# Optimization experiments

Hardware: AMD Instinct MI355X
Metric: run time of the kernel (lower is better)

Reference implementation:

```python
import jax, jax.numpy as jnp
import numpy as np

N_HEAD = 16


def setup_inputs() -> dict:
    key = jax.random.key(0)
    ks = jax.random.split(key, 5)
    B, T, D_IN, D = 2, 2048, 1152, 1024
    s_in = 1.0 / np.sqrt(D_IN)
    s_d = 1.0 / np.sqrt(D)
    return {
        "xp": jax.random.normal(ks[0], (B, T, D_IN), jnp.float32),
        "Wq": jax.random.normal(ks[1], (D_IN, D), jnp.float32) * s_in,
        "bq": jnp.zeros((D,), jnp.float32),
        "Wk": jax.random.normal(ks[2], (D_IN, D), jnp.float32) * s_in,
        "bk": jnp.zeros((D,), jnp.float32),
        "Wv": jax.random.normal(ks[3], (D_IN, D), jnp.float32) * s_in,
        "bv": jnp.zeros((D,), jnp.float32),
        "Wp": jax.random.normal(ks[4], (D, D), jnp.float32) * s_d,
        "bp": jnp.zeros((D,), jnp.float32),
    }


def reference(xp, Wq, bq, Wk, bk, Wv, bv, Wp, bp):
    B, T, _ = xp.shape
    D = Wq.shape[1]
    hd = D // N_HEAD  # head dim
    # q, k, v projections -> [B, H, T, hd]
    def split_heads(t):
        return t.reshape(B, T, N_HEAD, hd).transpose(0, 2, 1, 3)
    q = split_heads(xp @ Wq + bq)
    k = split_heads(xp @ Wk + bk)
    v = split_heads(xp @ Wv + bv)
    scale = 1.0 / np.sqrt(hd).astype(np.float32)
    att = jnp.einsum("bhqd,bhkd->bhqk", q, k) * scale  # [B,H,T,T]
    causal = jnp.tril(jnp.ones((T, T), bool))
    att = jnp.where(causal[None, None], att, -jnp.inf)
    att = jax.nn.softmax(att, axis=-1)
    y = jnp.einsum("bhqk,bhkd->bhqd", att, v)  # [B,H,T,hd]
    y = y.transpose(0, 2, 1, 3).reshape(B, T, D)
    return y @ Wp + bp
```

## Files before the change

### kernel.cpp

```cpp
#include <hip/hip_runtime.h>
#include <hip/hip_bf16.h>

typedef __attribute__((ext_vector_type(8))) short bf16x8;
typedef __attribute__((ext_vector_type(4))) float f32x4;
typedef __attribute__((ext_vector_type(2))) unsigned int u32x2;

__device__ __forceinline__ void gload_lds16(const void* g, void* l) {
    __builtin_amdgcn_global_load_lds(
        (const __attribute__((address_space(1))) unsigned int*)g,
        (__attribute__((address_space(3))) unsigned int*)l, 16, 0, 0);
}

__global__ void k_cvt_bf16(const float* __restrict__ x, __hip_bfloat16* __restrict__ o, int n8) {
    int i = blockIdx.x * 256 + threadIdx.x;
    if (i >= n8) return;
    const float4* xp = (const float4*)(x + (size_t)i * 8);
    float4 a = xp[0], b = xp[1];
    union { __hip_bfloat16 h[8]; uint4 u; } tu;
    tu.h[0] = __float2bfloat16(a.x); tu.h[1] = __float2bfloat16(a.y);
    tu.h[2] = __float2bfloat16(a.z); tu.h[3] = __float2bfloat16(a.w);
    tu.h[4] = __float2bfloat16(b.x); tu.h[5] = __float2bfloat16(b.y);
    tu.h[6] = __float2bfloat16(b.z); tu.h[7] = __float2bfloat16(b.w);
    *(uint4*)(o + (size_t)i * 8) = tu.u;
}

__global__ void k_tr(const float* __restrict__ src, __hip_bfloat16* __restrict__ dst, int K, int N) {
    __shared__ float tile[32][33];
    int n0 = blockIdx.x * 32, k0 = blockIdx.y * 32;
    int tx = threadIdx.x & 31, ty = threadIdx.x >> 5;
#pragma unroll
    for (int i = 0; i < 4; i++)
        tile[ty + i * 8][tx] = src[(size_t)(k0 + ty + i * 8) * N + n0 + tx];
    __syncthreads();
#pragma unroll
    for (int i = 0; i < 4; i++)
        dst[(size_t)(n0 + ty + i * 8) * K + k0 + tx] = __float2bfloat16(tile[tx][ty + i * 8]);
}

#define QSCALE 0.18033688011111204f

template <int EPI>
__global__ __launch_bounds__(256, 2) void k_gemm(
    const __hip_bfloat16* __restrict__ A, const __hip_bfloat16* __restrict__ Bt,
    int M, int N, int K,
    const float* __restrict__ b0, const float* __restrict__ b1, const float* __restrict__ b2,
    __hip_bfloat16* __restrict__ qb, __hip_bfloat16* __restrict__ kb, __hip_bfloat16* __restrict__ vb,
    float* __restrict__ outp)
{
    __shared__ __align__(16) __hip_bfloat16 As[128 * 64];
    __shared__ __align__(16) __hip_bfloat16 Bs[128 * 64];
    const int t = threadIdx.x;
    const int lane = t & 63, w = t >> 6;
    const int wr = w >> 1, wc = w & 1;
    const int r16 = lane & 15, kg = lane >> 4;
    const int m0 = blockIdx.x * 128, n0 = blockIdx.y * 128;
    f32x4 acc[4][4] = {};
    const int ksteps = K >> 6;
    for (int kt = 0; kt < ksteps; ++kt) {
        if (kt) __syncthreads();
        const int ks = kt * 64;
#pragma unroll
        for (int i = 0; i < 4; i++) {
            int ci = i * 256 + t;
            int row = ci >> 3, kc = (ci & 7) * 8;
            gload_lds16(A + (size_t)(m0 + row) * K + ks + kc, As + ci * 8);
        }
#pragma unroll
        for (int i = 0; i < 4; i++) {
            int ci = i * 256 + t;
            int row = ci >> 3, kc = (ci & 7) * 8;
            gload_lds16(Bt + (size_t)(n0 + row) * K + ks + kc, Bs + ci * 8);
        }
        __syncthreads();
#pragma unroll
        for (int c = 0; c < 2; c++) {
            bf16x8 af[4], bfr[4];
#pragma unroll
            for (int mi = 0; mi < 4; mi++)
                af[mi] = *(const bf16x8*)(As + (wr * 64 + mi * 16 + r16) * 64 + c * 32 + kg * 8);
#pragma unroll
            for (int ni = 0; ni < 4; ni++)
                bfr[ni] = *(const bf16x8*)(Bs + (wc * 64 + ni * 16 + r16) * 64 + c * 32 + kg * 8);
#pragma unroll
            for (int mi = 0; mi < 4; mi++)
#pragma unroll
                for (int ni = 0; ni < 4; ni++)
                    acc[mi][ni] = __builtin_amdgcn_mfma_f32_16x16x32_bf16(af[mi], bfr[ni], acc[mi][ni], 0, 0, 0);
        }
    }
#pragma unroll
    for (int mi = 0; mi < 4; mi++) {
#pragma unroll
        for (int ni = 0; ni < 4; ni++) {
#pragma unroll
            for (int j = 0; j < 4; j++) {
                int m = m0 + wr * 64 + mi * 16 + kg * 4 + j;
                int n = n0 + wc * 64 + ni * 16 + r16;
                float val = acc[mi][ni][j];
                if (EPI == 0) {
                    int proj = n >> 10, r = n & 1023;
                    int hh = r >> 6, dd = r & 63;
                    int bb = m >> 11, tt = m & 2047;
                    if (proj == 0) {
                        val = (val + b0[r]) * QSCALE;
                        qb[((size_t)(bb * 16 + hh) * 2048 + tt) * 64 + dd] = __float2bfloat16(val);
                    } else if (proj == 1) {
                        val += b1[r];
                        kb[((size_t)(bb * 16 + hh) * 2048 + tt) * 64 + dd] = __float2bfloat16(val);
                    } else {
                        val += b2[r];
                        vb[((size_t)(bb * 16 + hh) * 64 + dd) * 2048 + tt] = __float2bfloat16(val);
                    }
                } else {
                    outp[(size_t)m * N + n] = val + b0[n];
                }
            }
        }
    }
}

__global__ __launch_bounds__(256, 4) void k_attn(
    const __hip_bfloat16* __restrict__ qbuf,
    const __hip_bfloat16* __restrict__ kbuf,
    const __hip_bfloat16* __restrict__ vtbuf,
    __hip_bfloat16* __restrict__ y)
{
    __shared__ __align__(16) __hip_bfloat16 Kl[2][64 * 64];
    __shared__ __align__(16) __hip_bfloat16 Vl[2][64 * 64];
    __shared__ __align__(16) __hip_bfloat16 Pl[4 * 16 * 64];
    const int t = threadIdx.x, lane = t & 63, w = t >> 6;
    const int r16 = lane & 15, kg = lane >> 4;
    const int g = blockIdx.x;
    const int c4 = g >> 8, p = g & 255;
    const int bh = (p >> 5) * 4 + c4;
    const int rr = p & 31;
    const int qt = (c4 & 1) ? rr : 31 - rr;
    const int swr = (r16 & 7) << 3;
    const int q0 = qt * 64 + w * 16;
    const __hip_bfloat16* qp = qbuf + ((size_t)bh * 2048 + q0) * 64;
    bf16x8 qf0 = *(const bf16x8*)(qp + r16 * 64 + kg * 8);
    bf16x8 qf1 = *(const bf16x8*)(qp + r16 * 64 + 32 + kg * 8);
    f32x4 O[4] = {};
    float m_s = -3.0e38f, l_s = 0.f;
    const __hip_bfloat16* kb = kbuf + (size_t)bh * 2048 * 64;
    const __hip_bfloat16* vb = vtbuf + (size_t)bh * 64 * 2048;
    __hip_bfloat16* pw = Pl + w * 16 * 64;

    const int ci0 = t, ci1 = 256 + t;
    const int kr0 = ci0 >> 3, sc0 = ((ci0 & 7) * 8) ^ ((kr0 & 7) << 3);
    const int kr1 = ci1 >> 3, sc1 = ((ci1 & 7) * 8) ^ ((kr1 & 7) << 3);

    gload_lds16(kb + (size_t)kr0 * 64 + sc0, &Kl[0][ci0 * 8]);
    gload_lds16(kb + (size_t)kr1 * 64 + sc1, &Kl[0][ci1 * 8]);
    gload_lds16(vb + (size_t)kr0 * 2048 + sc0, &Vl[0][ci0 * 8]);
    gload_lds16(vb + (size_t)kr1 * 2048 + sc1, &Vl[0][ci1 * 8]);
    __syncthreads();

    for (int kt = 0; kt <= qt; ++kt) {
        const int cur = kt & 1;
        if (kt < qt) {
            const int kn = kt + 1;
            gload_lds16(kb + (size_t)kn * 4096 + (size_t)kr0 * 64 + sc0, &Kl[cur ^ 1][ci0 * 8]);
            gload_lds16(kb + (size_t)kn * 4096 + (size_t)kr1 * 64 + sc1, &Kl[cur ^ 1][ci1 * 8]);
            gload_lds16(vb + (size_t)kr0 * 2048 + kn * 64 + sc0, &Vl[cur ^ 1][ci0 * 8]);
            gload_lds16(vb + (size_t)kr1 * 2048 + kn * 64 + sc1, &Vl[cur ^ 1][ci1 * 8]);
        }
        const __hip_bfloat16* Klb = Kl[cur];
        const __hip_bfloat16* Vlb = Vl[cur];
        f32x4 S[4];
#pragma unroll
        for (int ct = 0; ct < 4; ct++) {
            f32x4 s = {};
            const int r = ct * 16 + r16;
            bf16x8 kf0 = *(const bf16x8*)(Klb + r * 64 + ((kg * 8) ^ swr));
            s = __builtin_amdgcn_mfma_f32_16x16x32_bf16(kf0, qf0, s, 0, 0, 0);
            bf16x8 kf1 = *(const bf16x8*)(Klb + r * 64 + ((32 + kg * 8) ^ swr));
            s = __builtin_amdgcn_mfma_f32_16x16x32_bf16(kf1, qf1, s, 0, 0, 0);
            S[ct] = s;
        }
        if (kt == qt) {
#pragma unroll
            for (int ct = 0; ct < 4; ct++)
#pragma unroll
                for (int j = 0; j < 4; j++)
                    if (ct * 16 + kg * 4 + j > w * 16 + r16) S[ct][j] = -3.0e38f;
        }
        float rmax = S[0][0];
#pragma unroll
        for (int ct = 0; ct < 4; ct++)
#pragma unroll
            for (int j = 0; j < 4; j++) rmax = fmaxf(rmax, S[ct][j]);
        rmax = fmaxf(rmax, __shfl_xor(rmax, 16));
        rmax = fmaxf(rmax, __shfl_xor(rmax, 32));
        if (__any(rmax > m_s + 8.0f)) {
            float mn = fmaxf(m_s, rmax);
            float alpha_s = exp2f(m_s - mn);
            m_s = mn;
            l_s *= alpha_s;
#pragma unroll
            for (int j = 0; j < 4; j++) {
                float aj = __shfl(alpha_s, (lane & 48) | (kg * 4 + j));
#pragma unroll
                for (int ot = 0; ot < 4; ot++) O[ot][j] *= aj;
            }
        }
        float rsum = 0.f;
#pragma unroll
        for (int ct = 0; ct < 4; ct++)
#pragma unroll
            for (int j = 0; j < 4; j++) {
                S[ct][j] = exp2f(S[ct][j] - m_s);
                rsum += S[ct][j];
            }
        rsum += __shfl_xor(rsum, 16);
        rsum += __shfl_xor(rsum, 32);
        l_s += rsum;
#pragma unroll
        for (int ct = 0; ct < 4; ct++) {
            union { __hip_bfloat16 h[4]; u32x2 u; } pk;
            pk.h[0] = __float2bfloat16(S[ct][0]);
            pk.h[1] = __float2bfloat16(S[ct][1]);
            pk.h[2] = __float2bfloat16(S[ct][2]);
            pk.h[3] = __float2bfloat16(S[ct][3]);
            const int col = (ct * 16 + kg * 4) ^ swr;
            *(u32x2*)(pw + r16 * 64 + col) = pk.u;
        }
        bf16x8 pa0 = *(const bf16x8*)(pw + r16 * 64 + ((kg * 8) ^ swr));
        bf16x8 pa1 = *(const bf16x8*)(pw + r16 * 64 + ((32 + kg * 8) ^ swr));
#pragma unroll
        for (int ot = 0; ot < 4; ot++) {
            const int vr = ot * 16 + r16;
            bf16x8 vf0 = *(const bf16x8*)(Vlb + vr * 64 + ((kg * 8) ^ swr));
            O[ot] = __builtin_amdgcn_mfma_f32_16x16x32_bf16(pa0, vf0, O[ot], 0, 0, 0);
            bf16x8 vf1 = *(const bf16x8*)(Vlb + vr * 64 + ((32 + kg * 8) ^ swr));
            O[ot] = __builtin_amdgcn_mfma_f32_16x16x32_bf16(pa1, vf1, O[ot], 0, 0, 0);
        }
        __syncthreads();
    }
    const int b = bh >> 4, h = bh & 15;
    float linv = 1.0f / l_s;
#pragma unroll
    for (int j = 0; j < 4; j++) {
        float ij = __shfl(linv, (lane & 48) | (kg * 4 + j));
        int qq = qt * 64 + w * 16 + kg * 4 + j;
#pragma unroll
        for (int ot = 0; ot < 4; ot++)
            y[((size_t)b * 2048 + qq) * 1024 + h * 64 + ot * 16 + r16] = __float2bfloat16(O[ot][j] * ij);
    }
}

extern "C" void kernel_launch(void* const* d_in, const int* in_sizes, int n_in,
                              void* d_out, int out_size, void* d_ws, size_t ws_size,
                              hipStream_t stream) {
    const float* xp = (const float*)d_in[0];
    const float* Wq = (const float*)d_in[1];
    const float* bq = (const float*)d_in[2];
    const float* Wk = (const float*)d_in[3];
    const float* bk = (const float*)d_in[4];
    const float* Wv = (const float*)d_in[5];
    const float* bv = (const float*)d_in[6];
    const float* Wp = (const float*)d_in[7];
    const float* bp = (const float*)d_in[8];
    float* out = (float*)d_out;

    char* ws = (char*)d_ws;
    __hip_bfloat16* xb     = (__hip_bfloat16*)(ws);
    __hip_bfloat16* Wqkv_t = (__hip_bfloat16*)(ws + 9437184);
    __hip_bfloat16* Wp_t   = (__hip_bfloat16*)(ws + 16515072);
    __hip_bfloat16* qb     = (__hip_bfloat16*)(ws + 18612224);
    __hip_bfloat16* kbv    = (__hip_bfloat16*)(ws + 27000832);
    __hip_bfloat16* vtb    = (__hip_bfloat16*)(ws + 35389440);
    __hip_bfloat16* yb     = (__hip_bfloat16*)(ws + 43778048);

    k_cvt_bf16<<<2304, 256, 0, stream>>>(xp, xb, 589824);
    dim3 trg(1024 / 32, 1152 / 32);
    k_tr<<<trg, 256, 0, stream>>>(Wq, Wqkv_t + (size_t)0 * 1024 * 1152, 1152, 1024);
    k_tr<<<trg, 256, 0, stream>>>(Wk, Wqkv_t + (size_t)1 * 1024 * 1152, 1152, 1024);
    k_tr<<<trg, 256, 0, stream>>>(Wv, Wqkv_t + (size_t)2 * 1024 * 1152, 1152, 1024);
    dim3 trg2(1024 / 32, 1024 / 32);
    k_tr<<<trg2, 256, 0, stream>>>(Wp, Wp_t, 1024, 1024);

    dim3 g1(4096 / 128, 3072 / 128);
    k_gemm<0><<<g1, 256, 0, stream>>>(xb, Wqkv_t, 4096, 3072, 1152, bq, bk, bv, qb, kbv, vtb, nullptr);
    k_attn<<<1024, 256, 0, stream>>>(qb, kbv, vtb, yb);
    dim3 g2(4096 / 128, 1024 / 128);
    k_gemm<1><<<g2, 256, 0, stream>>>(yb, Wp_t, 4096, 1024, 1024, bp, nullptr, nullptr,
                                      nullptr, nullptr, nullptr, out);
}
```

Baseline: 142.7 us.

## Switch attention to 32x32 MFMA with 128-row query tiles, double-buffer GEMM

Rewrites the attention kernel so each block handles 128 query rows, with each wave owning 32 rows. It uses 32x32x16 bf16 MFMA for both QK^T and PV, and rebuilds the P operand in registers with cross-lane shuffles instead of bouncing through LDS. Wave-level causal skipping replaces the per-tile loop bound, and the grid is halved to 512 blocks with launch bounds lowered to 2 blocks per CU. The projection GEMM also gains double-buffered LDS staging, so the next K tile loads while the current one is computed. The costs are more registers, doubled LDS, and more idle waves on the diagonal tiles.

```diff
diff --git a/kernel.cpp b/kernel.cpp
--- a/kernel.cpp
+++ b/kernel.cpp
@@ -3,12 +3,18 @@
 
 typedef __attribute__((ext_vector_type(8))) short bf16x8;
 typedef __attribute__((ext_vector_type(4))) float f32x4;
-typedef __attribute__((ext_vector_type(2))) unsigned int u32x2;
+typedef __attribute__((ext_vector_type(16))) float f32x16;
 
 __device__ __forceinline__ void gload_lds16(const void* g, void* l) {
     __builtin_amdgcn_global_load_lds(
         (const __attribute__((address_space(1))) unsigned int*)g,
         (__attribute__((address_space(3))) unsigned int*)l, 16, 0, 0);
+}
+
+__device__ __forceinline__ unsigned int pk2(float x, float y) {
+    union { __hip_bfloat16 h[2]; unsigned int u; } z;
+    z.h[0] = __float2bfloat16(x); z.h[1] = __float2bfloat16(y);
+    return z.u;
 }
 
 __global__ void k_cvt_bf16(const float* __restrict__ x, __hip_bfloat16* __restrict__ o, int n8) {
@@ -47,8 +53,8 @@
     __hip_bfloat16* __restrict__ qb, __hip_bfloat16* __restrict__ kb, __hip_bfloat16* __restrict__ vb,
     float* __restrict__ outp)
 {
-    __shared__ __align__(16) __hip_bfloat16 As[128 * 64];
-    __shared__ __align__(16) __hip_bfloat16 Bs[128 * 64];
+    __shared__ __align__(16) __hip_bfloat16 As[2][128 * 64];
+    __shared__ __align__(16) __hip_bfloat16 Bs[2][128 * 64];
     const int t = threadIdx.x;
     const int lane = t & 63, w = t >> 6;
     const int wr = w >> 1, wc = w & 1;
@@ -56,37 +62,45 @@
     const int m0 = blockIdx.x * 128, n0 = blockIdx.y * 128;
     f32x4 acc[4][4] = {};
     const int ksteps = K >> 6;
-    for (int kt = 0; kt < ksteps; ++kt) {
-        if (kt) __syncthreads();
+
+    auto stage = [&](int buf, int kt) {
         const int ks = kt * 64;
 #pragma unroll
         for (int i = 0; i < 4; i++) {
             int ci = i * 256 + t;
             int row = ci >> 3, kc = (ci & 7) * 8;
-            gload_lds16(A + (size_t)(m0 + row) * K + ks + kc, As + ci * 8);
+            gload_lds16(A + (size_t)(m0 + row) * K + ks + kc, &As[buf][ci * 8]);
         }
 #pragma unroll
         for (int i = 0; i < 4; i++) {
             int ci = i * 256 + t;
             int row = ci >> 3, kc = (ci & 7) * 8;
-            gload_lds16(Bt + (size_t)(n0 + row) * K + ks + kc, Bs + ci * 8);
-        }
-        __syncthreads();
+            gload_lds16(Bt + (size_t)(n0 + row) * K + ks + kc, &Bs[buf][ci * 8]);
+        }
+    };
+
+    stage(0, 0);
+    __syncthreads();
+    int cur = 0;
+    for (int kt = 0; kt < ksteps; ++kt) {
+        if (kt + 1 < ksteps) stage(cur ^ 1, kt + 1);
 #pragma unroll
         for (int c = 0; c < 2; c++) {
             bf16x8 af[4], bfr[4];
 #pragma unroll
             for (int mi = 0; mi < 4; mi++)
-                af[mi] = *(const bf16x8*)(As + (wr * 64 + mi * 16 + r16) * 64 + c * 32 + kg * 8);
+                af[mi] = *(const bf16x8*)(&As[cur][(wr * 64 + mi * 16 + r16) * 64 + c * 32 + kg * 8]);
 #pragma unroll
             for (int ni = 0; ni < 4; ni++)
-                bfr[ni] = *(const bf16x8*)(Bs + (wc * 64 + ni * 16 + r16) * 64 + c * 32 + kg * 8);
+                bfr[ni] = *(const bf16x8*)(&Bs[cur][(wc * 64 + ni * 16 + r16) * 64 + c * 32 + kg * 8]);
 #pragma unroll
             for (int mi = 0; mi < 4; mi++)
 #pragma unroll
                 for (int ni = 0; ni < 4; ni++)
                     acc[mi][ni] = __builtin_amdgcn_mfma_f32_16x16x32_bf16(af[mi], bfr[ni], acc[mi][ni], 0, 0, 0);
         }
+        __syncthreads();
+        cur ^= 1;
     }
 #pragma unroll
     for (int mi = 0; mi < 4; mi++) {
@@ -119,7 +133,7 @@
     }
 }
 
-__global__ __launch_bounds__(256, 4) void k_attn(
+__global__ __launch_bounds__(256, 2) void k_attn(
     const __hip_bfloat16* __restrict__ qbuf,
     const __hip_bfloat16* __restrict__ kbuf,
     const __hip_bfloat16* __restrict__ vtbuf,
@@ -127,24 +141,27 @@
 {
     __shared__ __align__(16) __hip_bfloat16 Kl[2][64 * 64];
     __shared__ __align__(16) __hip_bfloat16 Vl[2][64 * 64];
-    __shared__ __align__(16) __hip_bfloat16 Pl[4 * 16 * 64];
     const int t = threadIdx.x, lane = t & 63, w = t >> 6;
-    const int r16 = lane & 15, kg = lane >> 4;
+    const int l31 = lane & 31, hi = lane >> 5;
     const int g = blockIdx.x;
-    const int c4 = g >> 8, p = g & 255;
-    const int bh = (p >> 5) * 4 + c4;
-    const int rr = p & 31;
-    const int qt = (c4 & 1) ? rr : 31 - rr;
-    const int swr = (r16 & 7) << 3;
-    const int q0 = qt * 64 + w * 16;
-    const __hip_bfloat16* qp = qbuf + ((size_t)bh * 2048 + q0) * 64;
-    bf16x8 qf0 = *(const bf16x8*)(qp + r16 * 64 + kg * 8);
-    bf16x8 qf1 = *(const bf16x8*)(qp + r16 * 64 + 32 + kg * 8);
-    f32x4 O[4] = {};
+    const int c2 = g >> 8, p = g & 255;
+    const int bh = p & 31;
+    const int rr = p >> 5;
+    const int qt = c2 ? (15 - rr) : rr;
+    const int nt = 2 * qt + 2;
+    const int q0w = qt * 128 + w * 32;
+    const int swr = (l31 & 7) << 3;
+
+    const __hip_bfloat16* qp = qbuf + ((size_t)bh * 2048 + q0w + l31) * 64;
+    bf16x8 qf[4];
+#pragma unroll
+    for (int dt = 0; dt < 4; dt++)
+        qf[dt] = *(const bf16x8*)(qp + dt * 16 + hi * 8);
+
+    f32x16 O0 = {}, O1 = {};
     float m_s = -3.0e38f, l_s = 0.f;
     const __hip_bfloat16* kb = kbuf + (size_t)bh * 2048 * 64;
     const __hip_bfloat16* vb = vtbuf + (size_t)bh * 64 * 2048;
-    __hip_bfloat16* pw = Pl + w * 16 * 64;
 
     const int ci0 = t, ci1 = 256 + t;
     const int kr0 = ci0 >> 3, sc0 = ((ci0 & 7) * 8) ^ ((kr0 & 7) << 3);
@@ -156,96 +173,103 @@
     gload_lds16(vb + (size_t)kr1 * 2048 + sc1, &Vl[0][ci1 * 8]);
     __syncthreads();
 
-    for (int kt = 0; kt <= qt; ++kt) {
+    for (int kt = 0; kt < nt; ++kt) {
         const int cur = kt & 1;
-        if (kt < qt) {
+        if (kt + 1 < nt) {
             const int kn = kt + 1;
             gload_lds16(kb + (size_t)kn * 4096 + (size_t)kr0 * 64 + sc0, &Kl[cur ^ 1][ci0 * 8]);
             gload_lds16(kb + (size_t)kn * 4096 + (size_t)kr1 * 64 + sc1, &Kl[cur ^ 1][ci1 * 8]);
             gload_lds16(vb + (size_t)kr0 * 2048 + kn * 64 + sc0, &Vl[cur ^ 1][ci0 * 8]);
             gload_lds16(vb + (size_t)kr1 * 2048 + kn * 64 + sc1, &Vl[cur ^ 1][ci1 * 8]);
         }
-        const __hip_bfloat16* Klb = Kl[cur];
-        const __hip_bfloat16* Vlb = Vl[cur];
-        f32x4 S[4];
-#pragma unroll
-        for (int ct = 0; ct < 4; ct++) {
-            f32x4 s = {};
-            const int r = ct * 16 + r16;
-            bf16x8 kf0 = *(const bf16x8*)(Klb + r * 64 + ((kg * 8) ^ swr));
-            s = __builtin_amdgcn_mfma_f32_16x16x32_bf16(kf0, qf0, s, 0, 0, 0);
-            bf16x8 kf1 = *(const bf16x8*)(Klb + r * 64 + ((32 + kg * 8) ^ swr));
-            s = __builtin_amdgcn_mfma_f32_16x16x32_bf16(kf1, qf1, s, 0, 0, 0);
-            S[ct] = s;
-        }
-        if (kt == qt) {
-#pragma unroll
-            for (int ct = 0; ct < 4; ct++)
-#pragma unroll
-                for (int j = 0; j < 4; j++)
-                    if (ct * 16 + kg * 4 + j > w * 16 + r16) S[ct][j] = -3.0e38f;
-        }
-        float rmax = S[0][0];
-#pragma unroll
-        for (int ct = 0; ct < 4; ct++)
-#pragma unroll
-            for (int j = 0; j < 4; j++) rmax = fmaxf(rmax, S[ct][j]);
-        rmax = fmaxf(rmax, __shfl_xor(rmax, 16));
-        rmax = fmaxf(rmax, __shfl_xor(rmax, 32));
-        if (__any(rmax > m_s + 8.0f)) {
-            float mn = fmaxf(m_s, rmax);
-            float alpha_s = exp2f(m_s - mn);
-            m_s = mn;
-            l_s *= alpha_s;
-#pragma unroll
-            for (int j = 0; j < 4; j++) {
-                float aj = __shfl(alpha_s, (lane & 48) | (kg * 4 + j));
-#pragma unroll
-                for (int ot = 0; ot < 4; ot++) O[ot][j] *= aj;
-            }
-        }
-        float rsum = 0.f;
-#pragma unroll
-        for (int ct = 0; ct < 4; ct++)
-#pragma unroll
-            for (int j = 0; j < 4; j++) {
-                S[ct][j] = exp2f(S[ct][j] - m_s);
-                rsum += S[ct][j];
-            }
-        rsum += __shfl_xor(rsum, 16);
-        rsum += __shfl_xor(rsum, 32);
-        l_s += rsum;
-#pragma unroll
-        for (int ct = 0; ct < 4; ct++) {
-            union { __hip_bfloat16 h[4]; u32x2 u; } pk;
-            pk.h[0] = __float2bfloat16(S[ct][0]);
-            pk.h[1] = __float2bfloat16(S[ct][1]);
-            pk.h[2] = __float2bfloat16(S[ct][2]);
-            pk.h[3] = __float2bfloat16(S[ct][3]);
-            const int col = (ct * 16 + kg * 4) ^ swr;
-            *(u32x2*)(pw + r16 * 64 + col) = pk.u;
-        }
-        bf16x8 pa0 = *(const bf16x8*)(pw + r16 * 64 + ((kg * 8) ^ swr));
-        bf16x8 pa1 = *(const bf16x8*)(pw + r16 * 64 + ((32 + kg * 8) ^ swr));
-#pragma unroll
-        for (int ot = 0; ot < 4; ot++) {
-            const int vr = ot * 16 + r16;
-            bf16x8 vf0 = *(const bf16x8*)(Vlb + vr * 64 + ((kg * 8) ^ swr));
-            O[ot] = __builtin_amdgcn_mfma_f32_16x16x32_bf16(pa0, vf0, O[ot], 0, 0, 0);
-            bf16x8 vf1 = *(const bf16x8*)(Vlb + vr * 64 + ((32 + kg * 8) ^ swr));
-            O[ot] = __builtin_amdgcn_mfma_f32_16x16x32_bf16(pa1, vf1, O[ot], 0, 0, 0);
+        const int kbase = kt * 64;
+        if (kbase <= q0w + 31) {
+            const __hip_bfloat16* Klb = Kl[cur];
+            const __hip_bfloat16* Vlb = Vl[cur];
+            f32x16 s0 = {}, s1 = {};
+#pragma unroll
+            for (int dt = 0; dt < 4; dt++) {
+                bf16x8 ka = *(const bf16x8*)(Klb + l31 * 64 + ((dt * 16 + hi * 8) ^ swr));
+                s0 = __builtin_amdgcn_mfma_f32_32x32x16_bf16(ka, qf[dt], s0, 0, 0, 0);
+            }
+#pragma unroll
+            for (int dt = 0; dt < 4; dt++) {
+                bf16x8 kb2 = *(const bf16x8*)(Klb + (32 + l31) * 64 + ((dt * 16 + hi * 8) ^ swr));
+                s1 = __builtin_amdgcn_mfma_f32_32x32x16_bf16(kb2, qf[dt], s1, 0, 0, 0);
+            }
+            if (kbase + 63 > q0w) {
+                const int qg = q0w + l31;
+#pragma unroll
+                for (int r = 0; r < 16; ++r) {
+                    const int krow = (r & 3) + 8 * (r >> 2) + 4 * hi;
+                    if (kbase + krow > qg) s0[r] = -3.0e38f;
+                    if (kbase + 32 + krow > qg) s1[r] = -3.0e38f;
+                }
+            }
+            float rmax = s0[0];
+#pragma unroll
+            for (int r = 1; r < 16; ++r) rmax = fmaxf(rmax, s0[r]);
+#pragma unroll
+            for (int r = 0; r < 16; ++r) rmax = fmaxf(rmax, s1[r]);
+            rmax = fmaxf(rmax, __shfl_xor(rmax, 32));
+            if (__any(rmax > m_s + 8.0f)) {
+                const float mn = fmaxf(m_s, rmax);
+                const float al = exp2f(m_s - mn);
+                m_s = mn;
+                l_s *= al;
+#pragma unroll
+                for (int r = 0; r < 16; ++r) {
+                    const int qrow = (r & 3) + 8 * (r >> 2) + 4 * hi;
+                    const float ar = __shfl(al, qrow);
+                    O0[r] *= ar; O1[r] *= ar;
+                }
+            }
+            float rsum = 0.f;
+#pragma unroll
+            for (int r = 0; r < 16; ++r) { s0[r] = exp2f(s0[r] - m_s); rsum += s0[r]; }
+#pragma unroll
+            for (int r = 0; r < 16; ++r) { s1[r] = exp2f(s1[r] - m_s); rsum += s1[r]; }
+            rsum += __shfl_xor(rsum, 32);
+            l_s += rsum;
+            bf16x8 pa[4];
+#pragma unroll
+            for (int kt4 = 0; kt4 < 4; ++kt4) {
+                const f32x16& sc = (kt4 < 2) ? s0 : s1;
+                const int a8 = (kt4 & 1) * 8;
+                const unsigned int plo0 = pk2(sc[a8 + 0], sc[a8 + 1]);
+                const unsigned int plo1 = pk2(sc[a8 + 2], sc[a8 + 3]);
+                const unsigned int phi0 = pk2(sc[a8 + 4], sc[a8 + 5]);
+                const unsigned int phi1 = pk2(sc[a8 + 6], sc[a8 + 7]);
+                const unsigned int snd0 = hi ? plo0 : phi0;
+                const unsigned int snd1 = hi ? plo1 : phi1;
+                const unsigned int r0 = (unsigned int)__shfl_xor((int)snd0, 32);
+                const unsigned int r1 = (unsigned int)__shfl_xor((int)snd1, 32);
+                union { unsigned int u[4]; bf16x8 v; } fr;
+                fr.u[0] = hi ? r0 : plo0;
+                fr.u[1] = hi ? r1 : plo1;
+                fr.u[2] = hi ? phi0 : r0;
+                fr.u[3] = hi ? phi1 : r1;
+                pa[kt4] = fr.v;
+            }
+#pragma unroll
+            for (int kt4 = 0; kt4 < 4; ++kt4) {
+                bf16x8 vf0 = *(const bf16x8*)(Vlb + l31 * 64 + ((kt4 * 16 + hi * 8) ^ swr));
+                O0 = __builtin_amdgcn_mfma_f32_32x32x16_bf16(pa[kt4], vf0, O0, 0, 0, 0);
+                bf16x8 vf1 = *(const bf16x8*)(Vlb + (32 + l31) * 64 + ((kt4 * 16 + hi * 8) ^ swr));
+                O1 = __builtin_amdgcn_mfma_f32_32x32x16_bf16(pa[kt4], vf1, O1, 0, 0, 0);
+            }
         }
         __syncthreads();
     }
     const int b = bh >> 4, h = bh & 15;
-    float linv = 1.0f / l_s;
-#pragma unroll
-    for (int j = 0; j < 4; j++) {
-        float ij = __shfl(linv, (lane & 48) | (kg * 4 + j));
-        int qq = qt * 64 + w * 16 + kg * 4 + j;
-#pragma unroll
-        for (int ot = 0; ot < 4; ot++)
-            y[((size_t)b * 2048 + qq) * 1024 + h * 64 + ot * 16 + r16] = __float2bfloat16(O[ot][j] * ij);
+    const float linv = 1.0f / l_s;
+#pragma unroll
+    for (int r = 0; r < 16; ++r) {
+        const int qrow = (r & 3) + 8 * (r >> 2) + 4 * hi;
+        const float iv = __shfl(linv, qrow);
+        const size_t ro = ((size_t)b * 2048 + q0w + qrow) * 1024 + (size_t)h * 64;
+        y[ro + l31] = __float2bfloat16(O0[r] * iv);
+        y[ro + 32 + l31] = __float2bfloat16(O1[r] * iv);
     }
 }
 
@@ -282,7 +306,7 @@
 
     dim3 g1(4096 / 128, 3072 / 128);
     k_gemm<0><<<g1, 256, 0, stream>>>(xb, Wqkv_t, 4096, 3072, 1152, bq, bk, bv, qb, kbv, vtb, nullptr);
-    k_attn<<<1024, 256, 0, stream>>>(qb, kbv, vtb, yb);
+    k_attn<<<512, 256, 0, stream>>>(qb, kbv, vtb, yb);
     dim3 g2(4096 / 128, 1024 / 128);
     k_gemm<1><<<g2, 256, 0, stream>>>(yb, Wp_t, 4096, 1024, 1024, bp, nullptr, nullptr,
                                       nullptr, nullptr, nullptr, out);
```

Result: slower. 174.7 us (+22.4%).

## Keep attention P in registers, skip masked tiles, swizzle GEMM blocks, merge transposes

Applied to the files above, without the earlier changes.

The attention kernel no longer stages the softmax probabilities through LDS. It feeds them from registers into 16x16x16 bf16 MFMAs for the PV product, and waves skip diagonal tiles that are fully masked for their rows. MFMA regions are wrapped in s_setprio, the GEMM grids are flattened with an XCD-style block swizzle for cache locality, and the three QKV weight transposes become one launch. The register-fed PV path issues twice as many smaller MFMAs and narrower V loads in exchange for dropping the LDS round trip.

```diff
diff --git a/kernel.cpp b/kernel.cpp
--- a/kernel.cpp
+++ b/kernel.cpp
@@ -2,13 +2,23 @@
 #include <hip/hip_bf16.h>
 
 typedef __attribute__((ext_vector_type(8))) short bf16x8;
+typedef __attribute__((ext_vector_type(4))) short bf16x4;
 typedef __attribute__((ext_vector_type(4))) float f32x4;
-typedef __attribute__((ext_vector_type(2))) unsigned int u32x2;
 
 __device__ __forceinline__ void gload_lds16(const void* g, void* l) {
     __builtin_amdgcn_global_load_lds(
         (const __attribute__((address_space(1))) unsigned int*)g,
         (__attribute__((address_space(3))) unsigned int*)l, 16, 0, 0);
+}
+
+__device__ __forceinline__ f32x4 mfma_16x16x16(bf16x4 a, bf16x4 b, f32x4 c) {
+#if __has_builtin(__builtin_amdgcn_mfma_f32_16x16x16bf16_1k)
+    return __builtin_amdgcn_mfma_f32_16x16x16bf16_1k(a, b, c, 0, 0, 0);
+#else
+    f32x4 d = c;
+    asm volatile("v_mfma_f32_16x16x16_bf16 %0, %1, %2, %0" : "+v"(d) : "v"(a), "v"(b));
+    return d;
+#endif
 }
 
 __global__ void k_cvt_bf16(const float* __restrict__ x, __hip_bfloat16* __restrict__ o, int n8) {
@@ -24,6 +34,23 @@
     *(uint4*)(o + (size_t)i * 8) = tu.u;
 }
 
+__global__ void k_tr3(const float* __restrict__ s0, const float* __restrict__ s1,
+                      const float* __restrict__ s2, __hip_bfloat16* __restrict__ dst,
+                      int K, int N) {
+    __shared__ float tile[32][33];
+    const float* src = (blockIdx.z == 0) ? s0 : ((blockIdx.z == 1) ? s1 : s2);
+    __hip_bfloat16* d = dst + (size_t)blockIdx.z * N * K;
+    int n0 = blockIdx.x * 32, k0 = blockIdx.y * 32;
+    int tx = threadIdx.x & 31, ty = threadIdx.x >> 5;
+#pragma unroll
+    for (int i = 0; i < 4; i++)
+        tile[ty + i * 8][tx] = src[(size_t)(k0 + ty + i * 8) * N + n0 + tx];
+    __syncthreads();
+#pragma unroll
+    for (int i = 0; i < 4; i++)
+        d[(size_t)(n0 + ty + i * 8) * K + k0 + tx] = __float2bfloat16(tile[tx][ty + i * 8]);
+}
+
 __global__ void k_tr(const float* __restrict__ src, __hip_bfloat16* __restrict__ dst, int K, int N) {
     __shared__ float tile[32][33];
     int n0 = blockIdx.x * 32, k0 = blockIdx.y * 32;
@@ -45,7 +72,7 @@
     int M, int N, int K,
     const float* __restrict__ b0, const float* __restrict__ b1, const float* __restrict__ b2,
     __hip_bfloat16* __restrict__ qb, __hip_bfloat16* __restrict__ kb, __hip_bfloat16* __restrict__ vb,
-    float* __restrict__ outp)
+    float* __restrict__ outp, int mtiles)
 {
     __shared__ __align__(16) __hip_bfloat16 As[128 * 64];
     __shared__ __align__(16) __hip_bfloat16 Bs[128 * 64];
@@ -53,7 +80,10 @@
     const int lane = t & 63, w = t >> 6;
     const int wr = w >> 1, wc = w & 1;
     const int r16 = lane & 15, kg = lane >> 4;
-    const int m0 = blockIdx.x * 128, n0 = blockIdx.y * 128;
+    const int cpx = gridDim.x >> 3;
+    const int bid = blockIdx.x;
+    const int swz = (bid & 7) * cpx + (bid >> 3);
+    const int m0 = (swz % mtiles) * 128, n0 = (swz / mtiles) * 128;
     f32x4 acc[4][4] = {};
     const int ksteps = K >> 6;
     for (int kt = 0; kt < ksteps; ++kt) {
@@ -127,7 +157,6 @@
 {
     __shared__ __align__(16) __hip_bfloat16 Kl[2][64 * 64];
     __shared__ __align__(16) __hip_bfloat16 Vl[2][64 * 64];
-    __shared__ __align__(16) __hip_bfloat16 Pl[4 * 16 * 64];
     const int t = threadIdx.x, lane = t & 63, w = t >> 6;
     const int r16 = lane & 15, kg = lane >> 4;
     const int g = blockIdx.x;
@@ -144,7 +173,6 @@
     float m_s = -3.0e38f, l_s = 0.f;
     const __hip_bfloat16* kb = kbuf + (size_t)bh * 2048 * 64;
     const __hip_bfloat16* vb = vtbuf + (size_t)bh * 64 * 2048;
-    __hip_bfloat16* pw = Pl + w * 16 * 64;
 
     const int ci0 = t, ci1 = 256 + t;
     const int kr0 = ci0 >> 3, sc0 = ((ci0 & 7) * 8) ^ ((kr0 & 7) << 3);
@@ -165,87 +193,90 @@
             gload_lds16(vb + (size_t)kr0 * 2048 + kn * 64 + sc0, &Vl[cur ^ 1][ci0 * 8]);
             gload_lds16(vb + (size_t)kr1 * 2048 + kn * 64 + sc1, &Vl[cur ^ 1][ci1 * 8]);
         }
-        const __hip_bfloat16* Klb = Kl[cur];
-        const __hip_bfloat16* Vlb = Vl[cur];
-        f32x4 S[4];
-#pragma unroll
-        for (int ct = 0; ct < 4; ct++) {
-            f32x4 s = {};
-            const int r = ct * 16 + r16;
-            bf16x8 kf0 = *(const bf16x8*)(Klb + r * 64 + ((kg * 8) ^ swr));
-            s = __builtin_amdgcn_mfma_f32_16x16x32_bf16(kf0, qf0, s, 0, 0, 0);
-            bf16x8 kf1 = *(const bf16x8*)(Klb + r * 64 + ((32 + kg * 8) ^ swr));
-            s = __builtin_amdgcn_mfma_f32_16x16x32_bf16(kf1, qf1, s, 0, 0, 0);
-            S[ct] = s;
-        }
-        if (kt == qt) {
+        const int kbase = kt * 64;
+        if (kbase <= q0 + 15) {
+            const __hip_bfloat16* Klb = Kl[cur];
+            const __hip_bfloat16* Vlb = Vl[cur];
+            f32x4 S[4];
+            __builtin_amdgcn_s_setprio(1);
+#pragma unroll
+            for (int ct = 0; ct < 4; ct++) {
+                f32x4 s = {};
+                const int r = ct * 16 + r16;
+                bf16x8 kf0 = *(const bf16x8*)(Klb + r * 64 + ((kg * 8) ^ swr));
+                s = __builtin_amdgcn_mfma_f32_16x16x32_bf16(kf0, qf0, s, 0, 0, 0);
+                bf16x8 kf1 = *(const bf16x8*)(Klb + r * 64 + ((32 + kg * 8) ^ swr));
+                s = __builtin_amdgcn_mfma_f32_16x16x32_bf16(kf1, qf1, s, 0, 0, 0);
+                S[ct] = s;
+            }
+            __builtin_amdgcn_s_setprio(0);
+            if (kbase + 63 > q0) {
+#pragma unroll
+                for (int ct = 0; ct < 4; ct++)
+#pragma unroll
+                    for (int j = 0; j < 4; j++)
+                        if (kbase + ct * 16 + kg * 4 + j > q0 + r16) S[ct][j] = -3.0e38f;
+            }
+            float rmax = S[0][0];
 #pragma unroll
             for (int ct = 0; ct < 4; ct++)
 #pragma unroll
-                for (int j = 0; j < 4; j++)
-                    if (ct * 16 + kg * 4 + j > w * 16 + r16) S[ct][j] = -3.0e38f;
-        }
-        float rmax = S[0][0];
-#pragma unroll
-        for (int ct = 0; ct < 4; ct++)
-#pragma unroll
-            for (int j = 0; j < 4; j++) rmax = fmaxf(rmax, S[ct][j]);
-        rmax = fmaxf(rmax, __shfl_xor(rmax, 16));
-        rmax = fmaxf(rmax, __shfl_xor(rmax, 32));
-        if (__any(rmax > m_s + 8.0f)) {
-            float mn = fmaxf(m_s, rmax);
-            float alpha_s = exp2f(m_s - mn);
-            m_s = mn;
-            l_s *= alpha_s;
-#pragma unroll
-            for (int j = 0; j < 4; j++) {
-                float aj = __shfl(alpha_s, (lane & 48) | (kg * 4 + j));
-#pragma unroll
-                for (int ot = 0; ot < 4; ot++) O[ot][j] *= aj;
-            }
-        }
-        float rsum = 0.f;
-#pragma unroll
-        for (int ct = 0; ct < 4; ct++)
-#pragma unroll
-            for (int j = 0; j < 4; j++) {
-                S[ct][j] = exp2f(S[ct][j] - m_s);
-                rsum += S[ct][j];
-            }
-        rsum += __shfl_xor(rsum, 16);
-        rsum += __shfl_xor(rsum, 32);
-        l_s += rsum;
-#pragma unroll
-        for (int ct = 0; ct < 4; ct++) {
-            union { __hip_bfloat16 h[4]; u32x2 u; } pk;
-            pk.h[0] = __float2bfloat16(S[ct][0]);
-            pk.h[1] = __float2bfloat16(S[ct][1]);
-            pk.h[2] = __float2bfloat16(S[ct][2]);
-            pk.h[3] = __float2bfloat16(S[ct][3]);
-            const int col = (ct * 16 + kg * 4) ^ swr;
-            *(u32x2*)(pw + r16 * 64 + col) = pk.u;
-        }
-        bf16x8 pa0 = *(const bf16x8*)(pw + r16 * 64 + ((kg * 8) ^ swr));
-        bf16x8 pa1 = *(const bf16x8*)(pw + r16 * 64 + ((32 + kg * 8) ^ swr));
-#pragma unroll
-        for (int ot = 0; ot < 4; ot++) {
-            const int vr = ot * 16 + r16;
-            bf16x8 vf0 = *(const bf16x8*)(Vlb + vr * 64 + ((kg * 8) ^ swr));
-            O[ot] = __builtin_amdgcn_mfma_f32_16x16x32_bf16(pa0, vf0, O[ot], 0, 0, 0);
-            bf16x8 vf1 = *(const bf16x8*)(Vlb + vr * 64 + ((32 + kg * 8) ^ swr));
-            O[ot] = __builtin_amdgcn_mfma_f32_16x16x32_bf16(pa1, vf1, O[ot], 0, 0, 0);
+                for (int j = 0; j < 4; j++) rmax = fmaxf(rmax, S[ct][j]);
+            rmax = fmaxf(rmax, __shfl_xor(rmax, 16));
+            rmax = fmaxf(rmax, __shfl_xor(rmax, 32));
+            if (__any(rmax > m_s + 8.0f)) {
+                const float mn = fmaxf(m_s, rmax);
+                const float al = exp2f(m_s - mn);
+                m_s = mn;
+                l_s *= al;
+#pragma unroll
+                for (int j = 0; j < 4; j++) {
+                    const float aj = __shfl(al, kg * 4 + j);
+#pragma unroll
+                    for (int ot = 0; ot < 4; ot++) O[ot][j] *= aj;
+                }
+            }
+            float rsum = 0.f;
+#pragma unroll
+            for (int ct = 0; ct < 4; ct++)
+#pragma unroll
+                for (int j = 0; j < 4; j++) { S[ct][j] = exp2f(S[ct][j] - m_s); rsum += S[ct][j]; }
+            rsum += __shfl_xor(rsum, 16);
+            rsum += __shfl_xor(rsum, 32);
+            l_s += rsum;
+            bf16x4 pa[4];
+#pragma unroll
+            for (int ct = 0; ct < 4; ct++) {
+                union { __hip_bfloat16 h[4]; bf16x4 v; } pk;
+                pk.h[0] = __float2bfloat16(S[ct][0]);
+                pk.h[1] = __float2bfloat16(S[ct][1]);
+                pk.h[2] = __float2bfloat16(S[ct][2]);
+                pk.h[3] = __float2bfloat16(S[ct][3]);
+                pa[ct] = pk.v;
+            }
+            __builtin_amdgcn_s_setprio(1);
+#pragma unroll
+            for (int ot = 0; ot < 4; ot++) {
+                const int vrow = ot * 16 + r16;
+#pragma unroll
+                for (int ct = 0; ct < 4; ct++) {
+                    bf16x4 vf = *(const bf16x4*)(Vlb + vrow * 64 + ((ct * 16 + kg * 4) ^ ((vrow & 7) << 3)));
+                    O[ot] = mfma_16x16x16(pa[ct], vf, O[ot]);
+                }
+            }
+            __builtin_amdgcn_s_setprio(0);
         }
         __syncthreads();
     }
     const int b = bh >> 4, h = bh & 15;
-    float linv = 1.0f / l_s;
+    const float linv = 1.0f / l_s;
 #pragma unroll
     for (int j = 0; j < 4; j++) {
-        float ij = __shfl(linv, (lane & 48) | (kg * 4 + j));
-        int qq = qt * 64 + w * 16 + kg * 4 + j;
+        const float iv = __shfl(linv, kg * 4 + j);
+        const int qq = q0 + kg * 4 + j;
 #pragma unroll
         for (int ot = 0; ot < 4; ot++)
-            y[((size_t)b * 2048 + qq) * 1024 + h * 64 + ot * 16 + r16] = __float2bfloat16(O[ot][j] * ij);
+            y[((size_t)b * 2048 + qq) * 1024 + h * 64 + ot * 16 + r16] = __float2bfloat16(O[ot][j] * iv);
     }
 }
 
@@ -273,17 +304,14 @@
     __hip_bfloat16* yb     = (__hip_bfloat16*)(ws + 43778048);
 
     k_cvt_bf16<<<2304, 256, 0, stream>>>(xp, xb, 589824);
-    dim3 trg(1024 / 32, 1152 / 32);
-    k_tr<<<trg, 256, 0, stream>>>(Wq, Wqkv_t + (size_t)0 * 1024 * 1152, 1152, 1024);
-    k_tr<<<trg, 256, 0, stream>>>(Wk, Wqkv_t + (size_t)1 * 1024 * 1152, 1152, 1024);
-    k_tr<<<trg, 256, 0, stream>>>(Wv, Wqkv_t + (size_t)2 * 1024 * 1152, 1152, 1024);
+    dim3 trg3(1024 / 32, 1152 / 32, 3);
+    k_tr3<<<trg3, 256, 0, stream>>>(Wq, Wk, Wv, Wqkv_t, 1152, 1024);
     dim3 trg2(1024 / 32, 1024 / 32);
     k_tr<<<trg2, 256, 0, stream>>>(Wp, Wp_t, 1024, 1024);
 
-    dim3 g1(4096 / 128, 3072 / 128);
-    k_gemm<0><<<g1, 256, 0, stream>>>(xb, Wqkv_t, 4096, 3072, 1152, bq, bk, bv, qb, kbv, vtb, nullptr);
+    k_gemm<0><<<768, 256, 0, stream>>>(xb, Wqkv_t, 4096, 3072, 1152, bq, bk, bv, qb, kbv, vtb,
+                                       nullptr, 32);
     k_attn<<<1024, 256, 0, stream>>>(qb, kbv, vtb, yb);
-    dim3 g2(4096 / 128, 1024 / 128);
-    k_gemm<1><<<g2, 256, 0, stream>>>(yb, Wp_t, 4096, 1024, 1024, bp, nullptr, nullptr,
-                                      nullptr, nullptr, nullptr, out);
-}
+    k_gemm<1><<<256, 256, 0, stream>>>(yb, Wp_t, 4096, 1024, 1024, bp, nullptr, nullptr,
+                                       nullptr, nullptr, nullptr, out, 32);
+}
```

Measured after the change: 157.2 us. 10.1% more time.
